# Performance work log

Measured on AMD Instinct MI355X. Metric: run time of the kernel, lower is better.

## Reference

```python
import jax, jax.numpy as jnp
import numpy as np
import math

B, S, H, N = 1, 4096, 1024, 16
HN = H // N  # 64

def setup_inputs() -> dict:
    key = jax.random.key(0)
    k1, k2, k3 = jax.random.split(key, 3)
    hidden_states = jax.random.normal(k1, (B, S, H), dtype=jnp.float32)
    # lower-triangular causal mask, float {0,1}, broadcastable to [b,np,s,s]
    ltor_mask = jnp.tril(jnp.ones((1, 1, S, S), dtype=jnp.float32))
    w_qkv = jax.random.normal(k2, (3 * H, H), dtype=jnp.float32) * 0.02
    b_qkv = jnp.zeros((3 * H,), dtype=jnp.float32)
    w_dense = jax.random.normal(k3, (H, H), dtype=jnp.float32) * 0.02
    b_dense = jnp.zeros((H,), dtype=jnp.float32)
    return {"hidden_states": hidden_states, "ltor_mask": ltor_mask,
            "w_qkv": w_qkv, "b_qkv": b_qkv,
            "w_dense": w_dense, "b_dense": b_dense}

def reference(hidden_states, ltor_mask, w_qkv, b_qkv, w_dense, b_dense):
    b, s, h = hidden_states.shape
    # fused QKV projection: [b,s,3h]
    mixed = jnp.einsum('bsh,oh->bso', hidden_states, w_qkv) + b_qkv
    q, k, v = jnp.split(mixed, 3, axis=-1)
    # [b,s,h] -> [b,n,s,hn]
    def heads(t):
        return t.reshape(b, s, N, HN).transpose(0, 2, 1, 3)
    q, k, v = heads(q), heads(k), heads(v)
    # raw scores [b,n,s,s]
    scores = jnp.einsum('bnqd,bnkd->bnqk', q, k) / math.sqrt(HN)
    # multiplicative mask plus -10000 additive for masked positions
    scores = scores * ltor_mask - 10000.0 * (1.0 - ltor_mask)
    probs = jax.nn.softmax(scores, axis=-1)
    # attention dropout prob = 0.0 -> identity
    ctx = jnp.einsum('bnqk,bnkd->bnqd', probs, v)
    ctx = ctx.transpose(0, 2, 1, 3).reshape(b, s, h)
    out = jnp.einsum('bsh,oh->bso', ctx, w_dense) + b_dense
    # output dropout prob = 0.0 -> identity
    return out
```

## Files before the change

kernel.cpp:

```cpp
#include <hip/hip_runtime.h>
#include <hip/hip_bf16.h>

static constexpr int SEQ  = 4096;
static constexpr int HID  = 1024;
static constexpr int NHEAD = 16;
static constexpr int HDIM  = 64;
static constexpr int H3   = 3072;

typedef __attribute__((ext_vector_type(8))) __bf16 bf16x8;
typedef __attribute__((ext_vector_type(4))) float  f32x4;

__device__ __forceinline__ float bf2f(unsigned short u) {
    union { unsigned int u; float f; } v; v.u = ((unsigned int)u) << 16; return v.f;
}
__device__ __forceinline__ unsigned short f2bf(float f) {
    union { float f; unsigned int u; } v; v.f = f;
    unsigned int r = v.u + 0x7fffu + ((v.u >> 16) & 1u);
    return (unsigned short)(r >> 16);
}
__device__ __forceinline__ void gl_lds16(const unsigned short* g, unsigned short* l) {
    __builtin_amdgcn_global_load_lds(
        (const __attribute__((address_space(1))) void*)g,
        (__attribute__((address_space(3))) void*)l, 16, 0, 0);
}

struct Conv5 { const float* src[5]; unsigned short* dst[5]; };

__global__ __launch_bounds__(256) void convert5(Conv5 c) {
    constexpr int cnt[5]  = {4194304, 3145728, 3072, 1048576, 1024};
    constexpr int boff[5] = {0, 2048, 3584, 3586, 4098};
    const int b = blockIdx.x;
    int t = 0, rel = b;
#pragma unroll
    for (int k = 1; k < 5; ++k) if (b >= boff[k]) { t = k; rel = b - boff[k]; }
    const int base = rel * 2048 + threadIdx.x * 8;
    if (base >= cnt[t]) return;
    const float* s = c.src[t] + base;
    const float4 a = ((const float4*)s)[0];
    const float4 b2 = ((const float4*)s)[1];
    union { unsigned short v[8]; uint4 q; } u;
    u.v[0] = f2bf(a.x); u.v[1] = f2bf(a.y); u.v[2] = f2bf(a.z); u.v[3] = f2bf(a.w);
    u.v[4] = f2bf(b2.x); u.v[5] = f2bf(b2.y); u.v[6] = f2bf(b2.z); u.v[7] = f2bf(b2.w);
    *(uint4*)(c.dst[t] + base) = u.q;
}

template <int BM, int BN, int BK, typename OutT>
__global__ __launch_bounds__(256) void gemm_bt(
    const unsigned short* __restrict__ A, const unsigned short* __restrict__ B,
    const unsigned short* __restrict__ bias, OutT* __restrict__ C,
    int M, int N, int K)
{
    constexpr int MI  = BM / 32;
    constexpr int NI  = BN / 32;
    constexpr int KC  = BK / 32;
    constexpr int CB  = BK / 8;
    constexpr int LSH = (BK == 32) ? 2 : 3;
    constexpr int RPC = 64 >> LSH;

    const int tid  = threadIdx.x;
    const int wave = tid >> 6, lane = tid & 63;
    const int quad = lane >> 4, c16 = lane & 15;
    const int m0 = blockIdx.y * BM, n0 = blockIdx.x * BN;
    const int wr = wave >> 1, wc = wave & 1;

    __shared__ __align__(16) unsigned short sA[BM * BK];
    __shared__ __align__(16) unsigned short sB[BN * BK];

    f32x4 acc[MI][NI];
#pragma unroll
    for (int i = 0; i < MI; ++i)
#pragma unroll
        for (int j = 0; j < NI; ++j) acc[i][j] = {0.f, 0.f, 0.f, 0.f};

    const int sr = lane >> LSH;
    const int sc = ((lane & (CB - 1)) ^ (sr & (CB - 1))) * 8;

    for (int k0 = 0; k0 < K; k0 += BK) {
#pragma unroll
        for (int cc = 0; cc < BM / RPC / 4; ++cc) {
            const int rbase = cc * (4 * RPC) + wave * RPC;
            gl_lds16(A + (size_t)(m0 + rbase + sr) * K + k0 + sc, &sA[rbase * BK]);
        }
#pragma unroll
        for (int cc = 0; cc < BN / RPC / 4; ++cc) {
            const int rbase = cc * (4 * RPC) + wave * RPC;
            gl_lds16(B + (size_t)(n0 + rbase + sr) * K + k0 + sc, &sB[rbase * BK]);
        }
        __syncthreads();

#pragma unroll
        for (int kc = 0; kc < KC; ++kc) {
            bf16x8 af[MI], bfr[NI];
#pragma unroll
            for (int i = 0; i < MI; ++i) {
                const int ra = wr * (BM / 2) + i * 16 + c16;
                af[i] = *(const bf16x8*)&sA[ra * BK + (((kc * 4 + quad) ^ ra) & (CB - 1)) * 8];
            }
#pragma unroll
            for (int j = 0; j < NI; ++j) {
                const int rb = wc * (BN / 2) + j * 16 + c16;
                bfr[j] = *(const bf16x8*)&sB[rb * BK + (((kc * 4 + quad) ^ rb) & (CB - 1)) * 8];
            }
#pragma unroll
            for (int i = 0; i < MI; ++i)
#pragma unroll
                for (int j = 0; j < NI; ++j)
                    acc[i][j] = __builtin_amdgcn_mfma_f32_16x16x32_bf16(af[i], bfr[j], acc[i][j], 0, 0, 0);
        }
        __syncthreads();
    }

#pragma unroll
    for (int j = 0; j < NI; ++j) {
        const int col = n0 + wc * (BN / 2) + j * 16 + c16;
        const float bv = bf2f(bias[col]);
#pragma unroll
        for (int i = 0; i < MI; ++i) {
#pragma unroll
            for (int r = 0; r < 4; ++r) {
                const int row = m0 + wr * (BM / 2) + i * 16 + quad * 4 + r;
                const float v = acc[i][j][r] + bv;
                if constexpr (sizeof(OutT) == 2) C[(size_t)row * N + col] = (OutT)f2bf(v);
                else                             C[(size_t)row * N + col] = (OutT)v;
            }
        }
    }
}

__global__ __launch_bounds__(256) void transpose_v(
    const unsigned short* __restrict__ qkv, unsigned short* __restrict__ vt)
{
    const int n  = blockIdx.x >> 6;
    const int s0 = (blockIdx.x & 63) << 6;
    const int t  = threadIdx.x;
    __shared__ __align__(16) unsigned short tile[64][72];

#pragma unroll
    for (int p = 0; p < 2; ++p) {
        const int si = p * 32 + (t >> 3);
        const int d0 = (t & 7) * 8;
        const uint4 v = *(const uint4*)(qkv + (size_t)(s0 + si) * H3 + 2 * HID + n * HDIM + d0);
        *(uint4*)&tile[si][d0] = v;
    }
    __syncthreads();

    const int d    = t >> 2;
    const int soff = (t & 3) << 4;
    union { unsigned short s[16]; uint2 q2[4]; } buf;
#pragma unroll
    for (int i = 0; i < 16; ++i) buf.s[i] = tile[soff + i][d];
    const int k32 = soff & 32;
    const int tb4 = (soff & 16) >> 2;
    unsigned short* dst = vt + (size_t)(n * HDIM + d) * SEQ + s0 + k32 + tb4;
#pragma unroll
    for (int b = 0; b < 4; ++b)
        *(uint2*)(dst + b * 8) = buf.q2[b];
}

__global__ __launch_bounds__(128) void attn_causal(
    const unsigned short* __restrict__ qkv, const unsigned short* __restrict__ vt,
    unsigned short* __restrict__ ctx)
{
    const int bx = blockIdx.x;
    const int n  = bx & 15;
    const int z  = bx >> 4;
    const int qb = (z < 32) ? z : 95 - z;
    const int tid  = threadIdx.x;
    const int wave = tid >> 6, lane = tid & 63;
    const int quad = lane >> 4, c16 = lane & 15;

    __shared__ __align__(16) unsigned short smem[8192];
    unsigned short* smem_k = smem;
    unsigned short* smem_v = smem + 4096;

    const int qrow0 = qb * 64 + wave * 32;

    const float QS = 0.125f * 1.44269504f;
    bf16x8 qf[2][2];
#pragma unroll
    for (int wq = 0; wq < 2; ++wq)
#pragma unroll
        for (int kc = 0; kc < 2; ++kc) {
            bf16x8 q = *(const bf16x8*)(qkv + (size_t)(qrow0 + wq * 16 + c16) * H3 + n * HDIM + kc * 32 + quad * 8);
#pragma unroll
            for (int j = 0; j < 8; ++j) q[j] = (__bf16)((float)q[j] * QS);
            qf[wq][kc] = q;
        }

    f32x4 o[2][4];
#pragma unroll
    for (int wq = 0; wq < 2; ++wq)
#pragma unroll
        for (int dt = 0; dt < 4; ++dt) o[wq][dt] = {0.f, 0.f, 0.f, 0.f};
    float l_i[2] = {0.f, 0.f};

    const int srow8 = lane >> 3;
    const int scol8 = ((lane & 7) ^ (lane >> 3)) * 8;

    const int nkb = qb + 1;
    for (int kb = 0; kb < nkb; ++kb) {
        const int kv0 = kb * 64;
#pragma unroll
        for (int cc = 0; cc < 4; ++cc) {
            const int rbase = wave * 32 + cc * 8;
            gl_lds16(qkv + (size_t)(kv0 + rbase + srow8) * H3 + HID + n * HDIM + scol8,
                     &smem_k[rbase * 64]);
            gl_lds16(vt + (size_t)(n * HDIM + rbase + srow8) * SEQ + kv0 + scol8,
                     &smem_v[rbase * 64]);
        }
        __syncthreads();

        f32x4 s[2][4];
#pragma unroll
        for (int wq = 0; wq < 2; ++wq)
#pragma unroll
            for (int mt = 0; mt < 4; ++mt) s[wq][mt] = {0.f, 0.f, 0.f, 0.f};
#pragma unroll
        for (int mt = 0; mt < 4; ++mt) {
            const int row = mt * 16 + c16;
            const bf16x8 kf0 = *(const bf16x8*)&smem_k[row * 64 + ((quad)     ^ (row & 7)) * 8];
            const bf16x8 kf1 = *(const bf16x8*)&smem_k[row * 64 + ((4 + quad) ^ (row & 7)) * 8];
#pragma unroll
            for (int wq = 0; wq < 2; ++wq) {
                s[wq][mt] = __builtin_amdgcn_mfma_f32_16x16x32_bf16(kf0, qf[wq][0], s[wq][mt], 0, 0, 0);
                s[wq][mt] = __builtin_amdgcn_mfma_f32_16x16x32_bf16(kf1, qf[wq][1], s[wq][mt], 0, 0, 0);
            }
        }

#pragma unroll
        for (int wq = 0; wq < 2; ++wq) {
            if (kb == qb) {
                const int q_g = qrow0 + wq * 16 + c16;
#pragma unroll
                for (int mt = 0; mt < 4; ++mt)
#pragma unroll
                    for (int r = 0; r < 4; ++r) {
                        const int kv = kv0 + mt * 16 + quad * 4 + r;
                        if (kv > q_g) s[wq][mt][r] = -30000.0f;
                    }
            }
            float rs = 0.f;
#pragma unroll
            for (int mt = 0; mt < 4; ++mt)
#pragma unroll
                for (int r = 0; r < 4; ++r) {
                    const float p = __builtin_amdgcn_exp2f(s[wq][mt][r]);
                    s[wq][mt][r] = p;
                    rs += p;
                }
            l_i[wq] += rs;
        }

        bf16x8 pf[2][2];
#pragma unroll
        for (int wq = 0; wq < 2; ++wq)
#pragma unroll
            for (int kc = 0; kc < 2; ++kc) {
                union { __bf16 b[8]; bf16x8 v; } pp;
#pragma unroll
                for (int r = 0; r < 4; ++r) {
                    pp.b[r]     = (__bf16)s[wq][2 * kc][r];
                    pp.b[4 + r] = (__bf16)s[wq][2 * kc + 1][r];
                }
                pf[wq][kc] = pp.v;
            }

#pragma unroll
        for (int kc = 0; kc < 2; ++kc) {
#pragma unroll
            for (int dt = 0; dt < 4; ++dt) {
                const int row = dt * 16 + c16;
                const int c8 = (kc * 4 + quad) ^ (row & 7);
                const bf16x8 vf = *(const bf16x8*)&smem_v[row * 64 + c8 * 8];
#pragma unroll
                for (int wq = 0; wq < 2; ++wq)
                    o[wq][dt] = __builtin_amdgcn_mfma_f32_16x16x32_bf16(vf, pf[wq][kc], o[wq][dt], 0, 0, 0);
            }
        }
        __syncthreads();
    }

    float inv[2];
#pragma unroll
    for (int wq = 0; wq < 2; ++wq) {
        float l = l_i[wq];
        l += __shfl_xor(l, 16);
        l += __shfl_xor(l, 32);
        inv[wq] = 1.0f / l;
    }
    unsigned short* sc_ = smem + wave * 2304;
#pragma unroll
    for (int wq = 0; wq < 2; ++wq)
#pragma unroll
        for (int dt = 0; dt < 4; ++dt) {
            union { unsigned short u[4]; uint2 q2; } w;
#pragma unroll
            for (int r = 0; r < 4; ++r) w.u[r] = f2bf(o[wq][dt][r] * inv[wq]);
            *(uint2*)&sc_[(wq * 16 + c16) * 72 + dt * 16 + quad * 4] = w.q2;
        }
    const int qr = lane >> 1;
    const int xc = (lane & 1) * 32;
    unsigned short* dst = ctx + (size_t)(qrow0 + qr) * HID + n * HDIM + xc;
#pragma unroll
    for (int i = 0; i < 4; ++i)
        *(uint4*)(dst + i * 8) = *(const uint4*)&sc_[qr * 72 + xc + i * 8];
}

extern "C" void kernel_launch(void* const* d_in, const int* in_sizes, int n_in,
                              void* d_out, int out_size, void* d_ws, size_t ws_size,
                              hipStream_t stream)
{
    unsigned short* base = (unsigned short*)d_ws;

    unsigned short* hs_c = base;
    unsigned short* wq_c = hs_c + 4194304;
    unsigned short* bq_c = wq_c + 3145728;
    unsigned short* wd_c = bq_c + 3072;
    unsigned short* bd_c = wd_c + 1048576;
    unsigned short* qkv  = bd_c + 1024;
    unsigned short* vt   = qkv + (size_t)SEQ * H3;
    unsigned short* ctx  = hs_c;

    Conv5 c;
    c.src[0] = (const float*)d_in[0]; c.src[1] = (const float*)d_in[2];
    c.src[2] = (const float*)d_in[3]; c.src[3] = (const float*)d_in[4];
    c.src[4] = (const float*)d_in[5];
    c.dst[0] = hs_c; c.dst[1] = wq_c; c.dst[2] = bq_c; c.dst[3] = wd_c; c.dst[4] = bd_c;
    hipLaunchKernelGGL(convert5, dim3(4099), dim3(256), 0, stream, c);

    hipLaunchKernelGGL((gemm_bt<128, 128, 64, unsigned short>), dim3(H3 / 128, SEQ / 128), dim3(256), 0, stream,
                       hs_c, wq_c, bq_c, qkv, SEQ, H3, HID);
    hipLaunchKernelGGL(transpose_v, dim3(NHEAD * (SEQ / 64)), dim3(256), 0, stream, qkv, vt);
    hipLaunchKernelGGL(attn_causal, dim3(NHEAD * (SEQ / 64)), dim3(128), 0, stream, qkv, vt, ctx);
    hipLaunchKernelGGL((gemm_bt<64, 128, 64, float>), dim3(HID / 128, SEQ / 64), dim3(256), 0, stream,
                       ctx, wd_c, bd_c, (float*)d_out, SEQ, HID, HID);
}
```

Before: 259.0 us.

## Split causal attention KV range into chunks with separate reduction kernel

Attention is split flash-decoding style: each query block's KV range is divided into chunks of up to 16 key blocks, giving 160 work items per head instead of 64 uneven ones. Each chunk writes its normalized partial output and row sum, and a new reduce kernel combines them weighted by the sums. The aim is to balance load across CUs and shorten the critical path set by the longest causal rows. The cost is an extra launch plus partial-result traffic. The QKV GEMM K-tile is also reduced from 64 to 32.

```diff
diff --git a/kernel.cpp b/kernel.cpp
--- a/kernel.cpp
+++ b/kernel.cpp
@@ -157,14 +157,19 @@
         *(uint2*)(dst + b * 8) = buf.q2[b];
 }
 
-__global__ __launch_bounds__(128) void attn_causal(
+__global__ __launch_bounds__(128) void attn_partial(
     const unsigned short* __restrict__ qkv, const unsigned short* __restrict__ vt,
-    unsigned short* __restrict__ ctx)
-{
-    const int bx = blockIdx.x;
-    const int n  = bx & 15;
-    const int z  = bx >> 4;
-    const int qb = (z < 32) ? z : 95 - z;
+    unsigned short* __restrict__ partO, float* __restrict__ partl)
+{
+    const int slot = blockIdx.x;
+    const int n    = blockIdx.y;
+    int g = 0;
+#pragma unroll
+    for (int gg = 0; gg < 3; ++gg) if (slot >= 8 * (gg + 1) * (gg + 2)) g = gg + 1;
+    const int rel   = slot - 8 * g * (g + 1);
+    const int zq    = 16 * g + rel / (g + 1);
+    const int chunk = rel - (rel / (g + 1)) * (g + 1);
+
     const int tid  = threadIdx.x;
     const int wave = tid >> 6, lane = tid & 63;
     const int quad = lane >> 4, c16 = lane & 15;
@@ -173,7 +178,7 @@
     unsigned short* smem_k = smem;
     unsigned short* smem_v = smem + 4096;
 
-    const int qrow0 = qb * 64 + wave * 32;
+    const int qrow0 = zq * 64 + wave * 32;
 
     const float QS = 0.125f * 1.44269504f;
     bf16x8 qf[2][2];
@@ -197,8 +202,9 @@
     const int srow8 = lane >> 3;
     const int scol8 = ((lane & 7) ^ (lane >> 3)) * 8;
 
-    const int nkb = qb + 1;
-    for (int kb = 0; kb < nkb; ++kb) {
+    const int kb0 = chunk * 16;
+    const int kbe = min(kb0 + 16, zq + 1);
+    for (int kb = kb0; kb < kbe; ++kb) {
         const int kv0 = kb * 64;
 #pragma unroll
         for (int cc = 0; cc < 4; ++cc) {
@@ -229,7 +235,7 @@
 
 #pragma unroll
         for (int wq = 0; wq < 2; ++wq) {
-            if (kb == qb) {
+            if (kb == zq) {
                 const int q_g = qrow0 + wq * 16 + c16;
 #pragma unroll
                 for (int mt = 0; mt < 4; ++mt)
@@ -280,13 +286,20 @@
         __syncthreads();
     }
 
-    float inv[2];
+    const size_t base = (size_t)n * 160 + slot;
+    float inv[2], lval[2];
 #pragma unroll
     for (int wq = 0; wq < 2; ++wq) {
         float l = l_i[wq];
         l += __shfl_xor(l, 16);
         l += __shfl_xor(l, 32);
+        lval[wq] = l;
         inv[wq] = 1.0f / l;
+    }
+    if (quad == 0) {
+#pragma unroll
+        for (int wq = 0; wq < 2; ++wq)
+            partl[base * 64 + wave * 32 + wq * 16 + c16] = lval[wq];
     }
     unsigned short* sc_ = smem + wave * 2304;
 #pragma unroll
@@ -300,10 +313,47 @@
         }
     const int qr = lane >> 1;
     const int xc = (lane & 1) * 32;
-    unsigned short* dst = ctx + (size_t)(qrow0 + qr) * HID + n * HDIM + xc;
+    unsigned short* dst = partO + base * 4096 + (size_t)(wave * 32 + qr) * 64 + xc;
 #pragma unroll
     for (int i = 0; i < 4; ++i)
         *(uint4*)(dst + i * 8) = *(const uint4*)&sc_[qr * 72 + xc + i * 8];
+}
+
+__global__ __launch_bounds__(256) void attn_reduce(
+    const unsigned short* __restrict__ partO, const float* __restrict__ partl,
+    unsigned short* __restrict__ ctx)
+{
+    const int zq = blockIdx.x, n = blockIdx.y;
+    const int g  = zq >> 4;
+    const int nch = g + 1;
+    const int s0 = 8 * g * (g + 1) + (zq - 16 * g) * (g + 1);
+    const int tid = threadIdx.x;
+    const int q  = tid >> 2;
+    const int d0 = (tid & 3) * 16;
+
+    float acc[16];
+#pragma unroll
+    for (int i = 0; i < 16; ++i) acc[i] = 0.f;
+    float wsum = 0.f;
+
+    for (int c = 0; c < nch; ++c) {
+        const size_t base = (size_t)n * 160 + s0 + c;
+        const float w = partl[base * 64 + q];
+        const unsigned short* src = partO + base * 4096 + (size_t)q * 64 + d0;
+        union { unsigned short us[16]; uint4 q4[2]; } b;
+        b.q4[0] = *(const uint4*)src;
+        b.q4[1] = *(const uint4*)(src + 8);
+#pragma unroll
+        for (int i = 0; i < 16; ++i) acc[i] += w * bf2f(b.us[i]);
+        wsum += w;
+    }
+    const float inv = 1.0f / wsum;
+    union { unsigned short us[16]; uint4 q4[2]; } ob;
+#pragma unroll
+    for (int i = 0; i < 16; ++i) ob.us[i] = f2bf(acc[i] * inv);
+    unsigned short* dst = ctx + (size_t)(zq * 64 + q) * HID + n * HDIM + d0;
+    *(uint4*)dst       = ob.q4[0];
+    *(uint4*)(dst + 8) = ob.q4[1];
 }
 
 extern "C" void kernel_launch(void* const* d_in, const int* in_sizes, int n_in,
@@ -312,14 +362,16 @@
 {
     unsigned short* base = (unsigned short*)d_ws;
 
-    unsigned short* hs_c = base;
-    unsigned short* wq_c = hs_c + 4194304;
-    unsigned short* bq_c = wq_c + 3145728;
-    unsigned short* wd_c = bq_c + 3072;
-    unsigned short* bd_c = wd_c + 1048576;
-    unsigned short* qkv  = bd_c + 1024;
-    unsigned short* vt   = qkv + (size_t)SEQ * H3;
-    unsigned short* ctx  = hs_c;
+    unsigned short* hs_c  = base;
+    unsigned short* wq_c  = hs_c + 4194304;
+    unsigned short* bq_c  = wq_c + 3145728;
+    unsigned short* wd_c  = bq_c + 3072;
+    unsigned short* bd_c  = wd_c + 1048576;
+    unsigned short* qkv   = bd_c + 1024;
+    unsigned short* vt    = qkv + (size_t)SEQ * H3;
+    unsigned short* partO = vt + (size_t)NHEAD * HDIM * SEQ;
+    float*          partl = (float*)(partO + (size_t)2560 * 4096);
+    unsigned short* ctx   = hs_c;
 
     Conv5 c;
     c.src[0] = (const float*)d_in[0]; c.src[1] = (const float*)d_in[2];
@@ -328,10 +380,11 @@
     c.dst[0] = hs_c; c.dst[1] = wq_c; c.dst[2] = bq_c; c.dst[3] = wd_c; c.dst[4] = bd_c;
     hipLaunchKernelGGL(convert5, dim3(4099), dim3(256), 0, stream, c);
 
-    hipLaunchKernelGGL((gemm_bt<128, 128, 64, unsigned short>), dim3(H3 / 128, SEQ / 128), dim3(256), 0, stream,
+    hipLaunchKernelGGL((gemm_bt<128, 128, 32, unsigned short>), dim3(H3 / 128, SEQ / 128), dim3(256), 0, stream,
                        hs_c, wq_c, bq_c, qkv, SEQ, H3, HID);
     hipLaunchKernelGGL(transpose_v, dim3(NHEAD * (SEQ / 64)), dim3(256), 0, stream, qkv, vt);
-    hipLaunchKernelGGL(attn_causal, dim3(NHEAD * (SEQ / 64)), dim3(128), 0, stream, qkv, vt, ctx);
+    hipLaunchKernelGGL(attn_partial, dim3(160, NHEAD), dim3(128), 0, stream, qkv, vt, partO, partl);
+    hipLaunchKernelGGL(attn_reduce, dim3(SEQ / 64, NHEAD), dim3(256), 0, stream, partO, partl, ctx);
     hipLaunchKernelGGL((gemm_bt<64, 128, 64, float>), dim3(HID / 128, SEQ / 64), dim3(256), 0, stream,
                        ctx, wd_c, bd_c, (float*)d_out, SEQ, HID, HID);
 }
```

New measurement: 262.0 us. About the same (+1.2%).

## Fuse V transpose into QKV GEMM epilogue and split KV across waves

Applied to the files above, without the earlier changes.

The QKV GEMM epilogue now writes the V columns directly in transposed layout, so the separate transpose kernel is removed. The attention kernel grows to four waves: two query groups times two KV halves, processing 128 KV rows per iteration. Partial outputs and row sums are combined through shared memory at the end. The QKV GEMM K-tile also changes from 64 to 32. This cuts one launch and one pass over V, and adds parallelism per block, at the cost of more shared memory and a cross-wave reduction.

```diff
diff --git a/kernel.cpp b/kernel.cpp
--- a/kernel.cpp
+++ b/kernel.cpp
@@ -44,10 +44,11 @@
     *(uint4*)(c.dst[t] + base) = u.q;
 }
 
-template <int BM, int BN, int BK, typename OutT>
+template <int BM, int BN, int BK, typename OutT, bool VFUSE>
 __global__ __launch_bounds__(256) void gemm_bt(
     const unsigned short* __restrict__ A, const unsigned short* __restrict__ B,
     const unsigned short* __restrict__ bias, OutT* __restrict__ C,
+    unsigned short* __restrict__ vt,
     int M, int N, int K)
 {
     constexpr int MI  = BM / 32;
@@ -110,6 +111,28 @@
         __syncthreads();
     }
 
+    if constexpr (VFUSE) {
+        if (n0 >= 2048) {
+#pragma unroll
+            for (int j = 0; j < NI; ++j) {
+                const int col = n0 + wc * (BN / 2) + j * 16 + c16;
+                const float bv = bf2f(bias[col]);
+                const int d  = col - 2048;
+                unsigned short* vrow = vt + (size_t)d * SEQ;
+#pragma unroll
+                for (int i = 0; i < MI; ++i) {
+                    const int base32 = m0 + wr * (BM / 2) + (i >> 1) * 32;
+                    const int phys = base32 + 8 * quad + 4 * (i & 1);
+                    union { unsigned short u[4]; uint2 q2; } w;
+#pragma unroll
+                    for (int r = 0; r < 4; ++r) w.u[r] = f2bf(acc[i][j][r] + bv);
+                    *(uint2*)&vrow[phys] = w.q2;
+                }
+            }
+            return;
+        }
+    }
+
 #pragma unroll
     for (int j = 0; j < NI; ++j) {
         const int col = n0 + wc * (BN / 2) + j * 16 + c16;
@@ -127,53 +150,25 @@
     }
 }
 
-__global__ __launch_bounds__(256) void transpose_v(
-    const unsigned short* __restrict__ qkv, unsigned short* __restrict__ vt)
-{
-    const int n  = blockIdx.x >> 6;
-    const int s0 = (blockIdx.x & 63) << 6;
-    const int t  = threadIdx.x;
-    __shared__ __align__(16) unsigned short tile[64][72];
-
-#pragma unroll
-    for (int p = 0; p < 2; ++p) {
-        const int si = p * 32 + (t >> 3);
-        const int d0 = (t & 7) * 8;
-        const uint4 v = *(const uint4*)(qkv + (size_t)(s0 + si) * H3 + 2 * HID + n * HDIM + d0);
-        *(uint4*)&tile[si][d0] = v;
-    }
-    __syncthreads();
-
-    const int d    = t >> 2;
-    const int soff = (t & 3) << 4;
-    union { unsigned short s[16]; uint2 q2[4]; } buf;
-#pragma unroll
-    for (int i = 0; i < 16; ++i) buf.s[i] = tile[soff + i][d];
-    const int k32 = soff & 32;
-    const int tb4 = (soff & 16) >> 2;
-    unsigned short* dst = vt + (size_t)(n * HDIM + d) * SEQ + s0 + k32 + tb4;
-#pragma unroll
-    for (int b = 0; b < 4; ++b)
-        *(uint2*)(dst + b * 8) = buf.q2[b];
-}
-
-__global__ __launch_bounds__(128) void attn_causal(
+__global__ __launch_bounds__(256) void attn_causal(
     const unsigned short* __restrict__ qkv, const unsigned short* __restrict__ vt,
     unsigned short* __restrict__ ctx)
 {
     const int bx = blockIdx.x;
     const int n  = bx & 15;
-    const int z  = bx >> 4;
-    const int qb = (z < 32) ? z : 95 - z;
+    const int z0 = bx >> 4;
+    const int z  = (z0 < 32) ? z0 : 95 - z0;
     const int tid  = threadIdx.x;
     const int wave = tid >> 6, lane = tid & 63;
     const int quad = lane >> 4, c16 = lane & 15;
-
-    __shared__ __align__(16) unsigned short smem[8192];
+    const int qg  = wave & 1;
+    const int kvh = wave >> 1;
+
+    __shared__ __align__(16) unsigned short smem[16384];
     unsigned short* smem_k = smem;
-    unsigned short* smem_v = smem + 4096;
-
-    const int qrow0 = qb * 64 + wave * 32;
+    unsigned short* smem_v = smem + 8192;
+
+    const int qrow0 = z * 64 + qg * 32;
 
     const float QS = 0.125f * 1.44269504f;
     bf16x8 qf[2][2];
@@ -196,114 +191,140 @@
 
     const int srow8 = lane >> 3;
     const int scol8 = ((lane & 7) ^ (lane >> 3)) * 8;
-
-    const int nkb = qb + 1;
+    const int srow4 = lane >> 4;
+
+    const int nkb = (z + 2) >> 1;
     for (int kb = 0; kb < nkb; ++kb) {
-        const int kv0 = kb * 64;
+        const int kv0 = kb * 128;
 #pragma unroll
         for (int cc = 0; cc < 4; ++cc) {
-            const int rbase = wave * 32 + cc * 8;
-            gl_lds16(qkv + (size_t)(kv0 + rbase + srow8) * H3 + HID + n * HDIM + scol8,
-                     &smem_k[rbase * 64]);
-            gl_lds16(vt + (size_t)(n * HDIM + rbase + srow8) * SEQ + kv0 + scol8,
-                     &smem_v[rbase * 64]);
+            const int rb = wave * 32 + cc * 8;
+            gl_lds16(qkv + (size_t)(kv0 + rb + srow8) * H3 + HID + n * HDIM + scol8,
+                     &smem_k[rb * 64]);
+        }
+#pragma unroll
+        for (int cc = 0; cc < 4; ++cc) {
+            const int rb = wave * 16 + cc * 4;
+            const int sv = (((lane & 15) ^ ((cc * 4 + srow4) & 15))) * 8;
+            gl_lds16(vt + (size_t)(n * HDIM + rb + srow4) * SEQ + kv0 + sv,
+                     &smem_v[rb * 128]);
         }
         __syncthreads();
 
-        f32x4 s[2][4];
-#pragma unroll
-        for (int wq = 0; wq < 2; ++wq)
-#pragma unroll
-            for (int mt = 0; mt < 4; ++mt) s[wq][mt] = {0.f, 0.f, 0.f, 0.f};
-#pragma unroll
-        for (int mt = 0; mt < 4; ++mt) {
-            const int row = mt * 16 + c16;
-            const bf16x8 kf0 = *(const bf16x8*)&smem_k[row * 64 + ((quad)     ^ (row & 7)) * 8];
-            const bf16x8 kf1 = *(const bf16x8*)&smem_k[row * 64 + ((4 + quad) ^ (row & 7)) * 8];
+        const int kv0w = kv0 + kvh * 64;
+        if (kv0w <= qrow0 + 31) {
+            f32x4 s[2][4];
+#pragma unroll
+            for (int wq = 0; wq < 2; ++wq)
+#pragma unroll
+                for (int mt = 0; mt < 4; ++mt) s[wq][mt] = {0.f, 0.f, 0.f, 0.f};
+#pragma unroll
+            for (int mt = 0; mt < 4; ++mt) {
+                const int krow = kvh * 64 + mt * 16 + c16;
+                const bf16x8 kf0 = *(const bf16x8*)&smem_k[krow * 64 + ((quad)     ^ (krow & 7)) * 8];
+                const bf16x8 kf1 = *(const bf16x8*)&smem_k[krow * 64 + ((4 + quad) ^ (krow & 7)) * 8];
+#pragma unroll
+                for (int wq = 0; wq < 2; ++wq) {
+                    s[wq][mt] = __builtin_amdgcn_mfma_f32_16x16x32_bf16(kf0, qf[wq][0], s[wq][mt], 0, 0, 0);
+                    s[wq][mt] = __builtin_amdgcn_mfma_f32_16x16x32_bf16(kf1, qf[wq][1], s[wq][mt], 0, 0, 0);
+                }
+            }
+
 #pragma unroll
             for (int wq = 0; wq < 2; ++wq) {
-                s[wq][mt] = __builtin_amdgcn_mfma_f32_16x16x32_bf16(kf0, qf[wq][0], s[wq][mt], 0, 0, 0);
-                s[wq][mt] = __builtin_amdgcn_mfma_f32_16x16x32_bf16(kf1, qf[wq][1], s[wq][mt], 0, 0, 0);
-            }
-        }
-
+                if (kv0w + 63 > qrow0 + wq * 16) {
+                    const int q_g = qrow0 + wq * 16 + c16;
+#pragma unroll
+                    for (int mt = 0; mt < 4; ++mt)
+#pragma unroll
+                        for (int r = 0; r < 4; ++r) {
+                            const int kv = kv0w + mt * 16 + quad * 4 + r;
+                            if (kv > q_g) s[wq][mt][r] = -30000.0f;
+                        }
+                }
+                float rs = 0.f;
+#pragma unroll
+                for (int mt = 0; mt < 4; ++mt)
+#pragma unroll
+                    for (int r = 0; r < 4; ++r) {
+                        const float p = __builtin_amdgcn_exp2f(s[wq][mt][r]);
+                        s[wq][mt][r] = p;
+                        rs += p;
+                    }
+                l_i[wq] += rs;
+            }
+
+            bf16x8 pf[2][2];
+#pragma unroll
+            for (int wq = 0; wq < 2; ++wq)
+#pragma unroll
+                for (int kc = 0; kc < 2; ++kc) {
+                    union { __bf16 b[8]; bf16x8 v; } pp;
+#pragma unroll
+                    for (int r = 0; r < 4; ++r) {
+                        pp.b[r]     = (__bf16)s[wq][2 * kc][r];
+                        pp.b[4 + r] = (__bf16)s[wq][2 * kc + 1][r];
+                    }
+                    pf[wq][kc] = pp.v;
+                }
+
+#pragma unroll
+            for (int kc = 0; kc < 2; ++kc) {
+#pragma unroll
+                for (int dt = 0; dt < 4; ++dt) {
+                    const int vrow = dt * 16 + c16;
+                    const int pc8 = (kvh * 8 + kc * 4 + quad) ^ (vrow & 15);
+                    const bf16x8 vf = *(const bf16x8*)&smem_v[vrow * 128 + pc8 * 8];
+#pragma unroll
+                    for (int wq = 0; wq < 2; ++wq)
+                        o[wq][dt] = __builtin_amdgcn_mfma_f32_16x16x32_bf16(vf, pf[wq][kc], o[wq][dt], 0, 0, 0);
+                }
+            }
+        }
+        __syncthreads();
+    }
+
+#pragma unroll
+    for (int wq = 0; wq < 2; ++wq) {
+        l_i[wq] += __shfl_xor(l_i[wq], 16);
+        l_i[wq] += __shfl_xor(l_i[wq], 32);
+    }
+
+    float* cb = (float*)smem;
+    float* lb = (float*)(smem + 8704);
+    unsigned short* fb = smem + 8832;
+
+    if (kvh == 0) {
 #pragma unroll
         for (int wq = 0; wq < 2; ++wq) {
-            if (kb == qb) {
-                const int q_g = qrow0 + wq * 16 + c16;
-#pragma unroll
-                for (int mt = 0; mt < 4; ++mt)
-#pragma unroll
-                    for (int r = 0; r < 4; ++r) {
-                        const int kv = kv0 + mt * 16 + quad * 4 + r;
-                        if (kv > q_g) s[wq][mt][r] = -30000.0f;
-                    }
-            }
-            float rs = 0.f;
-#pragma unroll
-            for (int mt = 0; mt < 4; ++mt)
-#pragma unroll
-                for (int r = 0; r < 4; ++r) {
-                    const float p = __builtin_amdgcn_exp2f(s[wq][mt][r]);
-                    s[wq][mt][r] = p;
-                    rs += p;
-                }
-            l_i[wq] += rs;
-        }
-
-        bf16x8 pf[2][2];
-#pragma unroll
-        for (int wq = 0; wq < 2; ++wq)
-#pragma unroll
-            for (int kc = 0; kc < 2; ++kc) {
-                union { __bf16 b[8]; bf16x8 v; } pp;
-#pragma unroll
-                for (int r = 0; r < 4; ++r) {
-                    pp.b[r]     = (__bf16)s[wq][2 * kc][r];
-                    pp.b[4 + r] = (__bf16)s[wq][2 * kc + 1][r];
-                }
-                pf[wq][kc] = pp.v;
-            }
-
-#pragma unroll
-        for (int kc = 0; kc < 2; ++kc) {
+#pragma unroll
+            for (int dt = 0; dt < 4; ++dt)
+                *(f32x4*)&cb[(qg * 32 + wq * 16 + c16) * 68 + dt * 16 + quad * 4] = o[wq][dt];
+            if (quad == 0) lb[qg * 32 + wq * 16 + c16] = l_i[wq];
+        }
+    }
+    __syncthreads();
+    if (kvh == 1) {
+#pragma unroll
+        for (int wq = 0; wq < 2; ++wq) {
+            const float inv = 1.0f / (l_i[wq] + lb[qg * 32 + wq * 16 + c16]);
 #pragma unroll
             for (int dt = 0; dt < 4; ++dt) {
-                const int row = dt * 16 + c16;
-                const int c8 = (kc * 4 + quad) ^ (row & 7);
-                const bf16x8 vf = *(const bf16x8*)&smem_v[row * 64 + c8 * 8];
-#pragma unroll
-                for (int wq = 0; wq < 2; ++wq)
-                    o[wq][dt] = __builtin_amdgcn_mfma_f32_16x16x32_bf16(vf, pf[wq][kc], o[wq][dt], 0, 0, 0);
-            }
-        }
-        __syncthreads();
-    }
-
-    float inv[2];
-#pragma unroll
-    for (int wq = 0; wq < 2; ++wq) {
-        float l = l_i[wq];
-        l += __shfl_xor(l, 16);
-        l += __shfl_xor(l, 32);
-        inv[wq] = 1.0f / l;
-    }
-    unsigned short* sc_ = smem + wave * 2304;
-#pragma unroll
-    for (int wq = 0; wq < 2; ++wq)
-#pragma unroll
-        for (int dt = 0; dt < 4; ++dt) {
-            union { unsigned short u[4]; uint2 q2; } w;
-#pragma unroll
-            for (int r = 0; r < 4; ++r) w.u[r] = f2bf(o[wq][dt][r] * inv[wq]);
-            *(uint2*)&sc_[(wq * 16 + c16) * 72 + dt * 16 + quad * 4] = w.q2;
-        }
-    const int qr = lane >> 1;
-    const int xc = (lane & 1) * 32;
-    unsigned short* dst = ctx + (size_t)(qrow0 + qr) * HID + n * HDIM + xc;
-#pragma unroll
-    for (int i = 0; i < 4; ++i)
-        *(uint4*)(dst + i * 8) = *(const uint4*)&sc_[qr * 72 + xc + i * 8];
+                const f32x4 p = *(const f32x4*)&cb[(qg * 32 + wq * 16 + c16) * 68 + dt * 16 + quad * 4];
+                union { unsigned short u[4]; uint2 q2; } w;
+#pragma unroll
+                for (int r = 0; r < 4; ++r) w.u[r] = f2bf((o[wq][dt][r] + p[r]) * inv);
+                *(uint2*)&fb[(qg * 32 + wq * 16 + c16) * 72 + dt * 16 + quad * 4] = w.q2;
+            }
+        }
+    }
+    __syncthreads();
+
+    const int qr = tid >> 2;
+    const int xc = (tid & 3) * 16;
+    unsigned short* dst = ctx + (size_t)(z * 64 + qr) * HID + n * HDIM + xc;
+    *(uint4*)dst       = *(const uint4*)&fb[qr * 72 + xc];
+    *(uint4*)(dst + 8) = *(const uint4*)&fb[qr * 72 + xc + 8];
 }
 
 extern "C" void kernel_launch(void* const* d_in, const int* in_sizes, int n_in,
@@ -328,10 +349,12 @@
     c.dst[0] = hs_c; c.dst[1] = wq_c; c.dst[2] = bq_c; c.dst[3] = wd_c; c.dst[4] = bd_c;
     hipLaunchKernelGGL(convert5, dim3(4099), dim3(256), 0, stream, c);
 
-    hipLaunchKernelGGL((gemm_bt<128, 128, 64, unsigned short>), dim3(H3 / 128, SEQ / 128), dim3(256), 0, stream,
-                       hs_c, wq_c, bq_c, qkv, SEQ, H3, HID);
-    hipLaunchKernelGGL(transpose_v, dim3(NHEAD * (SEQ / 64)), dim3(256), 0, stream, qkv, vt);
-    hipLaunchKernelGGL(attn_causal, dim3(NHEAD * (SEQ / 64)), dim3(128), 0, stream, qkv, vt, ctx);
-    hipLaunchKernelGGL((gemm_bt<64, 128, 64, float>), dim3(HID / 128, SEQ / 64), dim3(256), 0, stream,
-                       ctx, wd_c, bd_c, (float*)d_out, SEQ, HID, HID);
-}
+    hipLaunchKernelGGL((gemm_bt<128, 128, 32, unsigned short, true>),
+                       dim3(H3 / 128, SEQ / 128), dim3(256), 0, stream,
+                       hs_c, wq_c, bq_c, qkv, vt, SEQ, H3, HID);
+    hipLaunchKernelGGL(attn_causal, dim3(NHEAD * (SEQ / 64)), dim3(256), 0, stream,
+                       qkv, vt, ctx);
+    hipLaunchKernelGGL((gemm_bt<64, 128, 64, float, false>),
+                       dim3(HID / 128, SEQ / 64), dim3(256), 0, stream,
+                       ctx, wd_c, bd_c, (float*)d_out, (unsigned short*)nullptr, SEQ, HID, HID);
+}
```

Result: faster. 247.3 us (-4.5%).
